# Performance work log

Hardware: AMD Instinct MI355X
Metric: run time of the kernel (lower is better)

Reference implementation:

```python
import jax, jax.numpy as jnp
import numpy as np

NGRAMS = (1, 2, 3, 4)


def _conv1d(x, W, b):
    # x: [B, S, E], W: [D, E, K], b: [D] -> [B, S-K+1, D] (valid conv, torch Conv1d)
    y = jax.lax.conv_general_dilated(
        x.transpose(0, 2, 1), W, window_strides=(1,), padding='VALID',
        dimension_numbers=('NCH', 'OIH', 'NCH'))
    return y.transpose(0, 2, 1) + b


def setup_inputs() -> dict:
    key = jax.random.key(0)
    ks = jax.random.split(key, 9)
    B, S, E, D = 64, 512, 256, 512
    inp = {'features': jax.random.normal(ks[0], (B, S, E), dtype=jnp.float32)}
    for i, n in enumerate(NGRAMS):
        fan_in = E * n
        inp[f'W{n}'] = jax.random.normal(ks[1 + 2 * i], (D, E, n), dtype=jnp.float32) / np.sqrt(fan_in)
        inp[f'b{n}'] = jax.random.normal(ks[2 + 2 * i], (D,), dtype=jnp.float32) * 0.01
    return inp


def reference(features, W1, b1, W2, b2, W3, b3, W4, b4):
    Ws = (W1, W2, W3, W4)
    bs = (b1, b2, b3, b4)
    # n-gram conv branches: branch g has kernel size NGRAMS[g] = g+1, length S - g
    feats = [_conv1d(features, W, b) for W, b in zip(Ws, bs)]
    B, S, E = features.shape
    flen = E  # faithful to original: features_len = features.shape[-1] (the embed dim)
    out = feats[0]  # unigram features, [B, S, D]
    i = jnp.arange(flen)
    add = jnp.zeros((B, flen, out.shape[-1]), out.dtype)
    # Original nested loops: out[:, i] += sum_{g=1}^{maxn-1} sum_{p=max(0,i-g+1)}^{min(i+1,L_g)-1} feats[g][:, p]
    # Computed here with per-branch prefix sums (exclusive) -> windowed sums.
    for g in range(1, max(NGRAMS)):
        y = feats[g]                      # [B, L, D], L = S - g
        L = y.shape[1]
        P = jnp.concatenate([jnp.zeros_like(y[:, :1]), jnp.cumsum(y, axis=1)], axis=1)  # [B, L+1, D]
        hi = jnp.minimum(i + 1, L)
        lo = jnp.minimum(jnp.maximum(0, i - g + 1), L)
        win = P[:, hi] - P[:, lo]         # [B, flen, D]
        add = add + jnp.where((hi > lo)[None, :, None], win, jnp.zeros_like(win))
    return out.at[:, :flen].add(add)
```

## Files before the change

kernel.cpp:

```cpp
#include <hip/hip_runtime.h>
#include <hip/hip_bf16.h>

#define EDIM 256
#define SDIM 512
#define BDIM 64
#define DDIM 512
#define SPAD 514

#define OFF_XP    0u
#define OFF_GINTB 16842752u
#define OFF_W1B   18415616u
#define OFF_G0T   18677760u
#define OFF_G1T   20774912u
#define OFF_BI    23396352u

typedef __attribute__((ext_vector_type(8))) __bf16 bf16x8;
typedef __attribute__((ext_vector_type(4))) float  f32x4;

__device__ __forceinline__ unsigned short f2bf(float f) {
    unsigned int u = __float_as_uint(f);
    u = (u + 0x7fffu + ((u >> 16) & 1u)) >> 16;
    return (unsigned short)u;
}

__global__ __launch_bounds__(256) void prep_all(
    const float* __restrict__ X,
    const float* __restrict__ W1, const float* __restrict__ b1,
    const float* __restrict__ W2, const float* __restrict__ b2,
    const float* __restrict__ W3, const float* __restrict__ b3,
    const float* __restrict__ W4, const float* __restrict__ b4,
    char* __restrict__ wsb)
{
    if (blockIdx.x < 8224) {
        unsigned short* Xp = (unsigned short*)(wsb + OFF_XP);
        int i = blockIdx.x * 256 + threadIdx.x;
        const int row = i >> 6;
        const int q   = i & 63;
        const int b   = row / SPAD;
        const int j   = row - b * SPAD;
        ushort4 v;
        if (j < 2) {
            v.x = v.y = v.z = v.w = 0;
        } else {
            const float4 f = *(const float4*)(X + ((size_t)(b * SDIM + j - 2)) * EDIM + q * 4);
            v.x = f2bf(f.x); v.y = f2bf(f.y); v.z = f2bf(f.z); v.w = f2bf(f.w);
        }
        *(ushort4*)(Xp + (size_t)row * EDIM + q * 4) = v;
        return;
    }

    const int d = blockIdx.x - 8224;
    const int e = threadIdx.x;
    const int de = d * EDIM + e;

    const float w1  = W1[de];
    const float w20 = W2[de * 2 + 0], w21 = W2[de * 2 + 1];
    const float w30 = W3[de * 3 + 0], w31 = W3[de * 3 + 1], w32 = W3[de * 3 + 2];
    const float w40 = W4[de * 4 + 0], w41 = W4[de * 4 + 1], w42 = W4[de * 4 + 2], w43 = W4[de * 4 + 3];

    unsigned short* Gi = (unsigned short*)(wsb + OFF_GINTB) + (size_t)d * 1536;
    Gi[0 * EDIM + e] = f2bf(w40);
    Gi[1 * EDIM + e] = f2bf(w30 + w40 + w41);
    Gi[2 * EDIM + e] = f2bf(w1 + w20 + w30 + w31 + w40 + w41 + w42);
    Gi[3 * EDIM + e] = f2bf(w21 + w31 + w32 + w41 + w42 + w43);
    Gi[4 * EDIM + e] = f2bf(w32 + w42 + w43);
    Gi[5 * EDIM + e] = f2bf(w43);

    ((unsigned short*)(wsb + OFF_W1B))[de] = f2bf(w1);

    float* G0t = (float*)(wsb + OFF_G0T);
    G0t[(0 * EDIM + e) * DDIM + d] = w1 + w20 + w30 + w40;
    G0t[(1 * EDIM + e) * DDIM + d] = w21 + w31 + w41;
    G0t[(2 * EDIM + e) * DDIM + d] = w32 + w42;
    G0t[(3 * EDIM + e) * DDIM + d] = w43;

    float* G1t = (float*)(wsb + OFF_G1T);
    G1t[(0 * EDIM + e) * DDIM + d] = w30 + w40;
    G1t[(1 * EDIM + e) * DDIM + d] = w1 + w20 + w30 + w31 + w40 + w41;
    G1t[(2 * EDIM + e) * DDIM + d] = w21 + w31 + w32 + w41 + w42;
    G1t[(3 * EDIM + e) * DDIM + d] = w32 + w42 + w43;
    G1t[(4 * EDIM + e) * DDIM + d] = w43;

    if (e == 0)
        ((float*)(wsb + OFF_BI))[d] = b1[d] + b2[d] + 2.0f * b3[d] + 3.0f * b4[d];
}

__global__ __launch_bounds__(256) void mega(
    const unsigned short* __restrict__ Xp,
    const char* __restrict__ wsb,
    const float* __restrict__ X,
    const float* __restrict__ b1, const float* __restrict__ b2,
    const float* __restrict__ b3, const float* __restrict__ b4,
    float* __restrict__ out)
{
    __shared__ __align__(16) char smem[16384];
    const int id  = blockIdx.x;
    const int tid = threadIdx.x;

    if (id >= 1024) {
        const int e  = id - 1024;
        const int b0 = (e >> 3) * 2;
        const int dg = (e & 7) * 64;
        float* xs = (float*)smem;
        float* pa = (float*)(smem + 10240);

        for (int i = tid; i < 2560; i += 256) {
            const int bb = (i < 1280) ? 0 : 1;
            const int kk = i - bb * 1280;
            xs[i] = X[(size_t)(b0 + bb) * (SDIM * EDIM) + kk];
        }
        __syncthreads();

        const float* G0t = (const float*)(wsb + OFF_G0T);
        const float* G1t = (const float*)(wsb + OFF_G1T);

        const int dl = tid & 63, ks = tid >> 6;
        const int d  = dg + dl;

        float a00 = 0.f, a10 = 0.f;
        float a01 = 0.f, a11 = 0.f;
#pragma unroll 4
        for (int k = ks * 256; k < ks * 256 + 256; ++k) {
            const float g = G0t[(size_t)k * DDIM + d];
            a00 += g * xs[k]; a10 += g * xs[1280 + k];
        }
#pragma unroll 4
        for (int k = ks * 320; k < ks * 320 + 320; ++k) {
            const float g = G1t[(size_t)k * DDIM + d];
            a01 += g * xs[k]; a11 += g * xs[1280 + k];
        }
        pa[(ks * 4 + 0) * 64 + dl] = a00;
        pa[(ks * 4 + 1) * 64 + dl] = a01;
        pa[(ks * 4 + 2) * 64 + dl] = a10;
        pa[(ks * 4 + 3) * 64 + dl] = a11;
        __syncthreads();

        const int c  = tid >> 6;
        const int dl2 = tid & 63;
        const int d2  = dg + dl2;
        float v = pa[(0 * 4 + c) * 64 + dl2] + pa[(1 * 4 + c) * 64 + dl2]
                + pa[(2 * 4 + c) * 64 + dl2] + pa[(3 * 4 + c) * 64 + dl2];
        const int s  = c & 1;
        const int bb = b0 + (c >> 1);
        const float bs = (s == 0) ? (b1[d2] + b2[d2] + b3[d2] + b4[d2])
                                  : (b1[d2] + b2[d2] + 2.f * b3[d2] + 2.f * b4[d2]);
        out[((size_t)bb * SDIM + s) * DDIM + d2] = v + bs;
        return;
    }

    const bool is_tail = id >= 512;
    const int  idx  = is_tail ? id - 512 : id;
    const int  row0 = (idx & 127) * 128;
    const int  col0 = (idx >> 7) * 128;
    const int  K     = is_tail ? 256 : 1536;
    const int  s_lo  = is_tail ? 256 : 0;
    const int  aoff  = is_tail ? 2 : 0;
    const unsigned short* Gbf = is_tail ? (const unsigned short*)(wsb + OFF_W1B)
                                        : (const unsigned short*)(wsb + OFF_GINTB);
    const float* bias = is_tail ? b1 : (const float*)(wsb + OFF_BI);

    unsigned short* Alds = (unsigned short*)smem;
    unsigned short* Blds = (unsigned short*)(smem + 8192);

    const int w = tid >> 6;
    const int l = tid & 63;

    const int sub = l >> 2;
    const int kb  = (l & 3) * 16;

    const int ra0 = row0 + 32 * w + sub;
    const int ra1 = ra0 + 16;
    const int ba0 = ra0 >> 8, sa0 = ra0 & 255;
    const int ba1 = ra1 >> 8, sa1 = ra1 & 255;
    const char* ga0 = (const char*)(Xp + ((size_t)(ba0 * SPAD + s_lo + sa0 + aoff)) * EDIM) + kb;
    const char* ga1 = (const char*)(Xp + ((size_t)(ba1 * SPAD + s_lo + sa1 + aoff)) * EDIM) + kb;
    const char* gb0 = (const char*)(Gbf + (size_t)(col0 + 32 * w + sub) * K) + kb;
    const char* gb1 = (const char*)(Gbf + (size_t)(col0 + 32 * w + 16 + sub) * K) + kb;

    unsigned short* la0 = Alds + (32 * w) * 32;
    unsigned short* la1 = Alds + (32 * w + 16) * 32;
    unsigned short* lb0 = Blds + (32 * w) * 32;
    unsigned short* lb1 = Blds + (32 * w + 16) * 32;

    const int wr  = (w >> 1) * 64;
    const int wc  = (w & 1) * 64;
    const int fm  = l & 15;
    const int fkb = (l >> 4) * 16;

    f32x4 acc[4][4] = {};
    const char* Ab = (const char*)Alds;
    const char* Bb = (const char*)Blds;

    const int nk = K >> 5;
    for (int kt = 0; kt < nk; ++kt) {
        __syncthreads();
        __builtin_amdgcn_global_load_lds((const __attribute__((address_space(1))) void*)ga0,
                                         (__attribute__((address_space(3))) void*)la0, 16, 0, 0);
        __builtin_amdgcn_global_load_lds((const __attribute__((address_space(1))) void*)ga1,
                                         (__attribute__((address_space(3))) void*)la1, 16, 0, 0);
        __builtin_amdgcn_global_load_lds((const __attribute__((address_space(1))) void*)gb0,
                                         (__attribute__((address_space(3))) void*)lb0, 16, 0, 0);
        __builtin_amdgcn_global_load_lds((const __attribute__((address_space(1))) void*)gb1,
                                         (__attribute__((address_space(3))) void*)lb1, 16, 0, 0);
        ga0 += 64; ga1 += 64; gb0 += 64; gb1 += 64;
        __syncthreads();

        bf16x8 af[4], bfr[4];
#pragma unroll
        for (int t = 0; t < 4; ++t) {
            af[t]  = *(const bf16x8*)(Ab + (wr + t * 16 + fm) * 64 + fkb);
            bfr[t] = *(const bf16x8*)(Bb + (wc + t * 16 + fm) * 64 + fkb);
        }
#pragma unroll
        for (int i = 0; i < 4; ++i)
#pragma unroll
            for (int j = 0; j < 4; ++j)
                acc[i][j] = __builtin_amdgcn_mfma_f32_16x16x32_bf16(af[i], bfr[j], acc[i][j], 0, 0, 0);
    }

    const int ocol = col0 + wc + fm;
    const int rq   = (l >> 4) * 4;
    float bv[4];
#pragma unroll
    for (int j = 0; j < 4; ++j) bv[j] = bias[ocol + j * 16];

#pragma unroll
    for (int i = 0; i < 4; ++i) {
#pragma unroll
        for (int r = 0; r < 4; ++r) {
            const int rr = row0 + wr + i * 16 + rq + r;
            const int ssl = rr & 255;
            if (!is_tail && ssl < 2) continue;
            const int bb = rr >> 8;
            const int ss = s_lo + ssl;
            float* op = out + ((size_t)(bb * SDIM + ss)) * DDIM + ocol;
#pragma unroll
            for (int j = 0; j < 4; ++j)
                op[j * 16] = acc[i][j][r] + bv[j];
        }
    }
}

extern "C" void kernel_launch(void* const* d_in, const int* in_sizes, int n_in,
                              void* d_out, int out_size, void* d_ws, size_t ws_size,
                              hipStream_t stream)
{
    const float* X  = (const float*)d_in[0];
    const float* W1 = (const float*)d_in[1];
    const float* b1 = (const float*)d_in[2];
    const float* W2 = (const float*)d_in[3];
    const float* b2 = (const float*)d_in[4];
    const float* W3 = (const float*)d_in[5];
    const float* b3 = (const float*)d_in[6];
    const float* W4 = (const float*)d_in[7];
    const float* b4 = (const float*)d_in[8];
    float* out = (float*)d_out;
    char*  wsb = (char*)d_ws;

    prep_all<<<dim3(8736), dim3(256), 0, stream>>>(X, W1, b1, W2, b2, W3, b3, W4, b4, wsb);

    mega<<<dim3(1280), dim3(256), 0, stream>>>(
        (const unsigned short*)(wsb + OFF_XP), wsb, X, b1, b2, b3, b4, out);
}
```

Before: 188.2 us.

## Replace boundary-row GEMV with small correction term and swizzle LDS layout

The separate fp32 path that computed output rows s=0,1 from transposed G0t/G1t matrices is removed. The main bf16 GEMM now also computes those rows, and a small per-batch correction (the W3/W4 terms that should not apply at the sequence start) is precomputed in prep and added in the epilogue. This drops the 5 MB transposed weight writes and 256 extra blocks. It also vectorizes the X-to-bf16 conversion to 8 elements per thread and XOR-swizzles the LDS k-offsets to reduce bank conflicts. Boundary rows now carry bf16 GEMM error plus an fp32 correction instead of pure fp32.

Result: slower. 260.3 us (+38.3%).

```diff
diff --git a/kernel.cpp b/kernel.cpp
--- a/kernel.cpp
+++ b/kernel.cpp
@@ -10,12 +10,17 @@
 #define OFF_XP    0u
 #define OFF_GINTB 16842752u
 #define OFF_W1B   18415616u
-#define OFF_G0T   18677760u
-#define OFF_G1T   20774912u
-#define OFF_BI    23396352u
+#define OFF_CORR  18677760u
+#define OFF_BI    18939904u
+
+#define CVT_BLOCKS  4112
+#define WB_BASE     4112
+#define CORR_BASE   4624
+#define PREP_BLOCKS 5136
 
 typedef __attribute__((ext_vector_type(8))) __bf16 bf16x8;
 typedef __attribute__((ext_vector_type(4))) float  f32x4;
+typedef __attribute__((ext_vector_type(8))) unsigned short ushort8v;
 
 __device__ __forceinline__ unsigned short f2bf(float f) {
     unsigned int u = __float_as_uint(f);
@@ -31,122 +36,100 @@
     const float* __restrict__ W4, const float* __restrict__ b4,
     char* __restrict__ wsb)
 {
-    if (blockIdx.x < 8224) {
+    const int tid = threadIdx.x;
+
+    if (blockIdx.x < CVT_BLOCKS) {
         unsigned short* Xp = (unsigned short*)(wsb + OFF_XP);
-        int i = blockIdx.x * 256 + threadIdx.x;
-        const int row = i >> 6;
-        const int q   = i & 63;
+        const int i   = blockIdx.x * 256 + tid;
+        const int row = i >> 5;
+        const int q   = i & 31;
         const int b   = row / SPAD;
         const int j   = row - b * SPAD;
-        ushort4 v;
+        ushort8v v;
         if (j < 2) {
-            v.x = v.y = v.z = v.w = 0;
+            v = (ushort8v)0;
         } else {
-            const float4 f = *(const float4*)(X + ((size_t)(b * SDIM + j - 2)) * EDIM + q * 4);
-            v.x = f2bf(f.x); v.y = f2bf(f.y); v.z = f2bf(f.z); v.w = f2bf(f.w);
-        }
-        *(ushort4*)(Xp + (size_t)row * EDIM + q * 4) = v;
+            const float* src = X + ((size_t)(b * SDIM + j - 2)) * EDIM + q * 8;
+            const float4 f0 = *(const float4*)(src);
+            const float4 f1 = *(const float4*)(src + 4);
+            v[0] = f2bf(f0.x); v[1] = f2bf(f0.y); v[2] = f2bf(f0.z); v[3] = f2bf(f0.w);
+            v[4] = f2bf(f1.x); v[5] = f2bf(f1.y); v[6] = f2bf(f1.z); v[7] = f2bf(f1.w);
+        }
+        *(ushort8v*)(Xp + (size_t)row * EDIM + q * 8) = v;
         return;
     }
 
-    const int d = blockIdx.x - 8224;
-    const int e = threadIdx.x;
-    const int de = d * EDIM + e;
-
-    const float w1  = W1[de];
-    const float w20 = W2[de * 2 + 0], w21 = W2[de * 2 + 1];
-    const float w30 = W3[de * 3 + 0], w31 = W3[de * 3 + 1], w32 = W3[de * 3 + 2];
-    const float w40 = W4[de * 4 + 0], w41 = W4[de * 4 + 1], w42 = W4[de * 4 + 2], w43 = W4[de * 4 + 3];
-
-    unsigned short* Gi = (unsigned short*)(wsb + OFF_GINTB) + (size_t)d * 1536;
-    Gi[0 * EDIM + e] = f2bf(w40);
-    Gi[1 * EDIM + e] = f2bf(w30 + w40 + w41);
-    Gi[2 * EDIM + e] = f2bf(w1 + w20 + w30 + w31 + w40 + w41 + w42);
-    Gi[3 * EDIM + e] = f2bf(w21 + w31 + w32 + w41 + w42 + w43);
-    Gi[4 * EDIM + e] = f2bf(w32 + w42 + w43);
-    Gi[5 * EDIM + e] = f2bf(w43);
-
-    ((unsigned short*)(wsb + OFF_W1B))[de] = f2bf(w1);
-
-    float* G0t = (float*)(wsb + OFF_G0T);
-    G0t[(0 * EDIM + e) * DDIM + d] = w1 + w20 + w30 + w40;
-    G0t[(1 * EDIM + e) * DDIM + d] = w21 + w31 + w41;
-    G0t[(2 * EDIM + e) * DDIM + d] = w32 + w42;
-    G0t[(3 * EDIM + e) * DDIM + d] = w43;
-
-    float* G1t = (float*)(wsb + OFF_G1T);
-    G1t[(0 * EDIM + e) * DDIM + d] = w30 + w40;
-    G1t[(1 * EDIM + e) * DDIM + d] = w1 + w20 + w30 + w31 + w40 + w41;
-    G1t[(2 * EDIM + e) * DDIM + d] = w21 + w31 + w32 + w41 + w42;
-    G1t[(3 * EDIM + e) * DDIM + d] = w32 + w42 + w43;
-    G1t[(4 * EDIM + e) * DDIM + d] = w43;
-
-    if (e == 0)
-        ((float*)(wsb + OFF_BI))[d] = b1[d] + b2[d] + 2.0f * b3[d] + 3.0f * b4[d];
+    if (blockIdx.x < CORR_BASE) {
+        const int d = blockIdx.x - WB_BASE;
+        const int e = tid;
+        const int de = d * EDIM + e;
+
+        const float w1  = W1[de];
+        const float w20 = W2[de * 2 + 0], w21 = W2[de * 2 + 1];
+        const float w30 = W3[de * 3 + 0], w31 = W3[de * 3 + 1], w32 = W3[de * 3 + 2];
+        const float w40 = W4[de * 4 + 0], w41 = W4[de * 4 + 1], w42 = W4[de * 4 + 2], w43 = W4[de * 4 + 3];
+
+        unsigned short* Gi = (unsigned short*)(wsb + OFF_GINTB) + (size_t)d * 1536;
+        Gi[0 * EDIM + e] = f2bf(w40);
+        Gi[1 * EDIM + e] = f2bf(w30 + w40 + w41);
+        Gi[2 * EDIM + e] = f2bf(w1 + w20 + w30 + w31 + w40 + w41 + w42);
+        Gi[3 * EDIM + e] = f2bf(w21 + w31 + w32 + w41 + w42 + w43);
+        Gi[4 * EDIM + e] = f2bf(w32 + w42 + w43);
+        Gi[5 * EDIM + e] = f2bf(w43);
+
+        ((unsigned short*)(wsb + OFF_W1B))[de] = f2bf(w1);
+
+        if (e == 0)
+            ((float*)(wsb + OFF_BI))[d] = b1[d] + b2[d] + 2.0f * b3[d] + 3.0f * b4[d];
+        return;
+    }
+
+    {
+        __shared__ float xs[768];
+        __shared__ float pa[2][4][64];
+        const int cb = blockIdx.x - CORR_BASE;
+        const int b  = cb >> 3;
+        const int dg = (cb & 7) * 64;
+
+        for (int i = tid; i < 768; i += 256)
+            xs[i] = X[(size_t)b * (SDIM * EDIM) + i];
+        __syncthreads();
+
+        const int dl = tid & 63, eq = tid >> 6;
+        const int d  = dg + dl;
+        const float* w3 = W3 + (size_t)d * 768;
+        const float* w4 = W4 + (size_t)d * 1024;
+
+        float a0 = 0.f, a1 = 0.f;
+        for (int e = eq * 64; e < eq * 64 + 64; ++e) {
+            const float w31 = w3[3 * e + 1], w32 = w3[3 * e + 2];
+            const float w41 = w4[4 * e + 1], w42 = w4[4 * e + 2], w43 = w4[4 * e + 3];
+            const float x0 = xs[e], x1 = xs[256 + e], x2 = xs[512 + e];
+            a0 += x0 * (w31 + w41 + w42) + x1 * (w32 + w42 + w43) + x2 * w43;
+            a1 += x0 * w41 + x1 * w42 + x2 * w43;
+        }
+        pa[0][eq][dl] = a0;
+        pa[1][eq][dl] = a1;
+        __syncthreads();
+
+        if (tid < 128) {
+            const int s = tid >> 6, d2l = tid & 63, d2 = dg + d2l;
+            const float v = pa[s][0][d2l] + pa[s][1][d2l] + pa[s][2][d2l] + pa[s][3][d2l];
+            const float bc = (s == 0) ? (b3[d2] + 2.f * b4[d2]) : b4[d2];
+            ((float*)(wsb + OFF_CORR))[((size_t)b * 2 + s) * DDIM + d2] = -v - bc;
+        }
+    }
 }
 
 __global__ __launch_bounds__(256) void mega(
     const unsigned short* __restrict__ Xp,
     const char* __restrict__ wsb,
-    const float* __restrict__ X,
-    const float* __restrict__ b1, const float* __restrict__ b2,
-    const float* __restrict__ b3, const float* __restrict__ b4,
+    const float* __restrict__ b1,
     float* __restrict__ out)
 {
     __shared__ __align__(16) char smem[16384];
     const int id  = blockIdx.x;
     const int tid = threadIdx.x;
-
-    if (id >= 1024) {
-        const int e  = id - 1024;
-        const int b0 = (e >> 3) * 2;
-        const int dg = (e & 7) * 64;
-        float* xs = (float*)smem;
-        float* pa = (float*)(smem + 10240);
-
-        for (int i = tid; i < 2560; i += 256) {
-            const int bb = (i < 1280) ? 0 : 1;
-            const int kk = i - bb * 1280;
-            xs[i] = X[(size_t)(b0 + bb) * (SDIM * EDIM) + kk];
-        }
-        __syncthreads();
-
-        const float* G0t = (const float*)(wsb + OFF_G0T);
-        const float* G1t = (const float*)(wsb + OFF_G1T);
-
-        const int dl = tid & 63, ks = tid >> 6;
-        const int d  = dg + dl;
-
-        float a00 = 0.f, a10 = 0.f;
-        float a01 = 0.f, a11 = 0.f;
-#pragma unroll 4
-        for (int k = ks * 256; k < ks * 256 + 256; ++k) {
-            const float g = G0t[(size_t)k * DDIM + d];
-            a00 += g * xs[k]; a10 += g * xs[1280 + k];
-        }
-#pragma unroll 4
-        for (int k = ks * 320; k < ks * 320 + 320; ++k) {
-            const float g = G1t[(size_t)k * DDIM + d];
-            a01 += g * xs[k]; a11 += g * xs[1280 + k];
-        }
-        pa[(ks * 4 + 0) * 64 + dl] = a00;
-        pa[(ks * 4 + 1) * 64 + dl] = a01;
-        pa[(ks * 4 + 2) * 64 + dl] = a10;
-        pa[(ks * 4 + 3) * 64 + dl] = a11;
-        __syncthreads();
-
-        const int c  = tid >> 6;
-        const int dl2 = tid & 63;
-        const int d2  = dg + dl2;
-        float v = pa[(0 * 4 + c) * 64 + dl2] + pa[(1 * 4 + c) * 64 + dl2]
-                + pa[(2 * 4 + c) * 64 + dl2] + pa[(3 * 4 + c) * 64 + dl2];
-        const int s  = c & 1;
-        const int bb = b0 + (c >> 1);
-        const float bs = (s == 0) ? (b1[d2] + b2[d2] + b3[d2] + b4[d2])
-                                  : (b1[d2] + b2[d2] + 2.f * b3[d2] + 2.f * b4[d2]);
-        out[((size_t)bb * SDIM + s) * DDIM + d2] = v + bs;
-        return;
-    }
 
     const bool is_tail = id >= 512;
     const int  idx  = is_tail ? id - 512 : id;
@@ -166,7 +149,7 @@
     const int l = tid & 63;
 
     const int sub = l >> 2;
-    const int kb  = (l & 3) * 16;
+    const int kb  = (((l & 3) ^ ((sub & 3) ^ ((sub >> 2) & 3)))) * 16;
 
     const int ra0 = row0 + 32 * w + sub;
     const int ra1 = ra0 + 16;
@@ -185,7 +168,7 @@
     const int wr  = (w >> 1) * 64;
     const int wc  = (w & 1) * 64;
     const int fm  = l & 15;
-    const int fkb = (l >> 4) * 16;
+    const int fkb = (((l >> 4) ^ ((fm & 3) ^ ((fm >> 2) & 3)))) * 16;
 
     f32x4 acc[4][4] = {};
     const char* Ab = (const char*)Alds;
@@ -218,6 +201,7 @@
                 acc[i][j] = __builtin_amdgcn_mfma_f32_16x16x32_bf16(af[i], bfr[j], acc[i][j], 0, 0, 0);
     }
 
+    const float* corr = (const float*)(wsb + OFF_CORR);
     const int ocol = col0 + wc + fm;
     const int rq   = (l >> 4) * 4;
     float bv[4];
@@ -228,15 +212,21 @@
     for (int i = 0; i < 4; ++i) {
 #pragma unroll
         for (int r = 0; r < 4; ++r) {
-            const int rr = row0 + wr + i * 16 + rq + r;
+            const int rr  = row0 + wr + i * 16 + rq + r;
             const int ssl = rr & 255;
-            if (!is_tail && ssl < 2) continue;
-            const int bb = rr >> 8;
-            const int ss = s_lo + ssl;
+            const int bb  = rr >> 8;
+            const int ss  = s_lo + ssl;
             float* op = out + ((size_t)(bb * SDIM + ss)) * DDIM + ocol;
-#pragma unroll
-            for (int j = 0; j < 4; ++j)
-                op[j * 16] = acc[i][j][r] + bv[j];
+            if (!is_tail && ssl < 2) {
+                const float* cp = corr + ((size_t)bb * 2 + ssl) * DDIM + ocol;
+#pragma unroll
+                for (int j = 0; j < 4; ++j)
+                    op[j * 16] = acc[i][j][r] + bv[j] + cp[j * 16];
+            } else {
+#pragma unroll
+                for (int j = 0; j < 4; ++j)
+                    op[j * 16] = acc[i][j][r] + bv[j];
+            }
         }
     }
 }
@@ -257,8 +247,8 @@
     float* out = (float*)d_out;
     char*  wsb = (char*)d_ws;
 
-    prep_all<<<dim3(8736), dim3(256), 0, stream>>>(X, W1, b1, W2, b2, W3, b3, W4, b4, wsb);
-
-    mega<<<dim3(1280), dim3(256), 0, stream>>>(
-        (const unsigned short*)(wsb + OFF_XP), wsb, X, b1, b2, b3, b4, out);
-}
+    prep_all<<<dim3(PREP_BLOCKS), dim3(256), 0, stream>>>(X, W1, b1, W2, b2, W3, b3, W4, b4, wsb);
+
+    mega<<<dim3(1024), dim3(256), 0, stream>>>(
+        (const unsigned short*)(wsb + OFF_XP), wsb, b1, out);
+}
```
